# Kernel optimization log

Hardware: AMD Instinct MI355X
Metric: run time of the kernel (lower is better)

The kernel has to match this reference:

```python
import jax, jax.numpy as jnp
import numpy as np

B, S, HID = 2, 2048, 2048
NH, NKV, D = 32, 8, 64
G = NH // NKV
THETA = 150000.0


def rotate_half(x):
    x1, x2 = x[..., : D // 2], x[..., D // 2 :]
    return jnp.concatenate([-x2, x1], axis=-1)


def setup_inputs() -> dict:
    key = jax.random.key(0)
    ks = jax.random.split(key, 10)
    sc = 0.02
    return {
        "hidden_states": jax.random.normal(ks[0], (B, S, HID), jnp.float32),
        "position_ids": jnp.arange(S, dtype=jnp.int64 if jax.config.jax_enable_x64 else jnp.int32),
        "wq": jax.random.normal(ks[1], (HID, NH * D), jnp.float32) * sc,
        "bq": jax.random.normal(ks[2], (NH * D,), jnp.float32) * sc,
        "wk": jax.random.normal(ks[3], (HID, NKV * D), jnp.float32) * sc,
        "bk": jax.random.normal(ks[4], (NKV * D,), jnp.float32) * sc,
        "wv": jax.random.normal(ks[5], (HID, NKV * D), jnp.float32) * sc,
        "bv": jax.random.normal(ks[6], (NKV * D,), jnp.float32) * sc,
        "wo": jax.random.normal(ks[7], (NH * D, HID), jnp.float32) * sc,
        "bo": jax.random.normal(ks[8], (HID,), jnp.float32) * sc,
    }


def reference(hidden_states, position_ids, wq, bq, wk, bk, wv, bv, wo, bo):
    # projections: [B,S,NH,D] / [B,S,NKV,D] -> head-major
    q = (hidden_states @ wq + bq).reshape(B, S, NH, D).transpose(0, 2, 1, 3)   # [B,NH,S,D]
    k = (hidden_states @ wk + bk).reshape(B, S, NKV, D).transpose(0, 2, 1, 3)  # [B,NKV,S,D]
    v = (hidden_states @ wv + bv).reshape(B, S, NKV, D).transpose(0, 2, 1, 3)

    # HF RoPE: inv_freq over even dims, freqs duplicated across the two halves
    inv_freq = 1.0 / (THETA ** (jnp.arange(0, D, 2, dtype=jnp.float32) / D))   # [D/2]
    freqs = position_ids.astype(jnp.float32)[:, None] * inv_freq[None, :]      # [S,D/2]
    emb = jnp.concatenate([freqs, freqs], axis=-1)                             # [S,D]
    cos = jnp.cos(emb)[None, None]  # [1,1,S,D]
    sin = jnp.sin(emb)[None, None]
    q = q * cos + rotate_half(q) * sin
    k = k * cos + rotate_half(k) * sin

    # GQA: group query heads by kv head instead of repeat_interleave on K/V
    qg = q.reshape(B, NKV, G, S, D)
    scores = jnp.einsum("bkgsd,bktd->bkgst", qg, k) / jnp.sqrt(jnp.float32(D))  # [B,NKV,G,S,S]
    attn = jax.nn.softmax(scores, axis=-1)
    out = jnp.einsum("bkgst,bktd->bkgsd", attn, v)                              # [B,NKV,G,S,D]
    out = out.reshape(B, NH, S, D).transpose(0, 2, 1, 3).reshape(B, S, NH * D)  # [B,S,NH*D]
    return out @ wo + bo
```

## Files before the change

kernel.cpp:

```cpp
#include <hip/hip_runtime.h>
#include <hip/hip_bf16.h>
#include <math.h>

#define B_   2
#define S_   2048
#define HID_ 2048
#define NH_  32
#define NKV_ 8
#define D_   64
#define G_   (NH_/NKV_)
#define M_   (B_*S_)

typedef __hip_bfloat16 bf16;
typedef short bf16x8 __attribute__((ext_vector_type(8)));
typedef float f32x4  __attribute__((ext_vector_type(4)));
typedef unsigned short u16x4 __attribute__((ext_vector_type(4)));

__device__ inline unsigned short f2bfu(float f){
    __hip_bfloat16 h = __float2bfloat16(f);
    return __builtin_bit_cast(unsigned short, h);
}

__device__ __forceinline__ float fexp2(float x){
#if __has_builtin(__builtin_amdgcn_exp2f)
    return __builtin_amdgcn_exp2f(x);
#else
    return exp2f(x);
#endif
}

__device__ __forceinline__ void async16(const void* g, void* l) {
    __builtin_amdgcn_global_load_lds(
        (const __attribute__((address_space(1))) unsigned int*)g,
        (__attribute__((address_space(3))) unsigned int*)l, 16, 0, 0);
}

#define SWZ(r, c) ((c) ^ (((r) & 7) << 3))

#define S_BARRIER() asm volatile("s_barrier" ::: "memory")
__device__ __forceinline__ void vmwait4(){ asm volatile("s_waitcnt vmcnt(4)" ::: "memory"); }
__device__ __forceinline__ void vmwait0(){ asm volatile("s_waitcnt vmcnt(0)" ::: "memory"); }

__device__ __forceinline__ void wtrans_body(
    const float* __restrict__ s0, int N0,
    const float* __restrict__ s1, int N1,
    const float* __restrict__ s2, int N2,
    bf16* __restrict__ dst, int K, int bx, int by,
    unsigned short* __restrict__ tbuf)
{
    unsigned short (*t)[65] = (unsigned short (*)[65])tbuf;
    const int ntile = bx * 64, ktile = by * 64;
    const float* src; int nloc, Nseg;
    if (ntile < N0)           { src = s0; nloc = ntile;           Nseg = N0; }
    else if (ntile < N0 + N1) { src = s1; nloc = ntile - N0;      Nseg = N1; }
    else                      { src = s2; nloc = ntile - N0 - N1; Nseg = N2; }
    const int r  = threadIdx.x >> 4;
    const int c4 = (threadIdx.x & 15) * 4;
    #pragma unroll
    for (int p = 0; p < 4; p++) {
        const int k = p * 16 + r;
        const float4 f = *(const float4*)(src + (size_t)(ktile + k) * Nseg + nloc + c4);
        t[k][c4+0] = f2bfu(f.x); t[k][c4+1] = f2bfu(f.y);
        t[k][c4+2] = f2bfu(f.z); t[k][c4+3] = f2bfu(f.w);
    }
    __syncthreads();
    #pragma unroll
    for (int p = 0; p < 4; p++) {
        const int n = p * 16 + r;
        u16x4 u = { t[c4+0][n], t[c4+1][n], t[c4+2][n], t[c4+3][n] };
        *(u16x4*)((unsigned short*)dst + (size_t)(ntile + n) * K + ktile + c4) = u;
    }
}

__global__ __launch_bounds__(256) void prep_k(
    const float* __restrict__ hs, bf16* __restrict__ hs_b,
    const float* __restrict__ wq, const float* __restrict__ wk,
    const float* __restrict__ wv, bf16* __restrict__ wqkvT,
    const int* __restrict__ pos, float* __restrict__ ctab,
    float* __restrict__ stab)
{
    __shared__ unsigned short tbuf[64 * 65];
    const int bid = blockIdx.x;
    if (bid < 4096) {
        const int i = (bid * 256 + threadIdx.x) * 8;
        const float4 a = *(const float4*)(hs + i);
        const float4 b = *(const float4*)(hs + i + 4);
        uint4 u;
        u.x = (unsigned)f2bfu(a.x) | ((unsigned)f2bfu(a.y) << 16);
        u.y = (unsigned)f2bfu(a.z) | ((unsigned)f2bfu(a.w) << 16);
        u.z = (unsigned)f2bfu(b.x) | ((unsigned)f2bfu(b.y) << 16);
        u.w = (unsigned)f2bfu(b.z) | ((unsigned)f2bfu(b.w) << 16);
        *(uint4*)((unsigned short*)hs_b + i) = u;
    } else if (bid < 5632) {
        const int t = bid - 4096;
        wtrans_body(wq, 2048, wk, 512, wv, 512, wqkvT, HID_,
                    t % 48, t / 48, tbuf);
    } else {
        const int idx = (bid - 5632) * 256 + threadIdx.x;
        const int s = idx >> 5, i = idx & 31;
        const int is64 = (pos[1] == 0);
        const int p = is64 ? pos[2 * s] : pos[s];
        const double inv = exp(-(double)i * (log(150000.0) / 32.0));
        const double f = (double)p * inv;
        ctab[idx] = (float)cos(f);
        stab[idx] = (float)sin(f);
    }
}

__device__ __forceinline__ void slab64(
    const bf16* __restrict__ g, int grow0, int k0,
    unsigned short* lds, int wave, int lane)
{
    const int rr = wave * 8 + (lane >> 3);
    const int cc = ((lane & 7) ^ (lane >> 3)) * 8;
    async16(g + (size_t)(grow0 + rr) * 2048 + k0 + cc, lds + wave * 512);
}

template<int MODE, int BM>
__global__ __launch_bounds__(512, 2) void gemm8p_k(
    const bf16* __restrict__ A, const bf16* __restrict__ WT,
    const float* __restrict__ b0, const float* __restrict__ b1,
    const float* __restrict__ b2,
    bf16* __restrict__ Cq, bf16* __restrict__ Ck, bf16* __restrict__ Cv,
    float* __restrict__ Cout,
    const float* __restrict__ ctab, const float* __restrict__ stab)
{
    constexpr int MT = BM / 32;
    constexpr int PM = MT / 4;
    constexpr int LA = BM * 64;
    constexpr int LB = 256 * 64;
    constexpr int NT = 32;
    __shared__ unsigned short sA[2 * LA];
    __shared__ unsigned short sB[2 * LB];

    const int tid  = threadIdx.x;
    const int wave = tid >> 6, lane = tid & 63;
    const int li   = lane & 15, lj = lane >> 4;
    const int wm   = wave >> 2, wn = wave & 3;

    const int nbx = gridDim.x, nby = gridDim.y;
    const int lin = blockIdx.y * nbx + blockIdx.x;
    const int qq  = (nbx * nby) >> 3;
    const int logical = (lin & 7) * qq + (lin >> 3);
    const int m0 = (logical % nby) * BM;
    const int n0 = (logical / nby) * 256;
    const int swz = li & 7;

    f32x4 acc[MT][4];
    #pragma unroll
    for (int i = 0; i < MT; ++i)
        #pragma unroll
        for (int j = 0; j < 4; ++j)
            acc[i][j] = (f32x4){0.f, 0.f, 0.f, 0.f};

    bf16x8 bfr[4][2];

    auto stageA = [&](int t, int r0) {
        unsigned short* l = sA + (t & 1) * LA + r0 * 64;
        const int k0 = (t & (NT - 1)) * 64;
        slab64(A, m0 + r0,      k0, l,           wave, lane);
        slab64(A, m0 + r0 + 64, k0, l + 64 * 64, wave, lane);
    };
    auto stageB = [&](int t, int r0) {
        unsigned short* l = sB + (t & 1) * LB + r0 * 64;
        const int k0 = (t & (NT - 1)) * 64;
        slab64(WT, n0 + r0,      k0, l,           wave, lane);
        slab64(WT, n0 + r0 + 64, k0, l + 64 * 64, wave, lane);
    };
    auto ldB = [&](int tb) {
        const unsigned short* base = sB + tb * LB;
        #pragma unroll
        for (int nt = 0; nt < 4; ++nt)
            #pragma unroll
            for (int ks = 0; ks < 2; ++ks)
                bfr[nt][ks] = *(const bf16x8*)
                    &base[(wn * 64 + nt * 16 + li) * 64 + ((ks * 4 + lj) ^ swz) * 8];
    };
    auto ldA = [&](int tb, int q, bf16x8 (*af)[2]) {
        const unsigned short* base = sA + tb * LA;
        #pragma unroll
        for (int m = 0; m < PM; ++m)
            #pragma unroll
            for (int ks = 0; ks < 2; ++ks)
                af[m][ks] = *(const bf16x8*)
                    &base[(wm * (BM / 2) + (q * PM + m) * 16 + li) * 64
                          + ((ks * 4 + lj) ^ swz) * 8];
    };
    auto mfma_q = [&](int q, bf16x8 (*af)[2]) {
        __builtin_amdgcn_s_setprio(1);
        #pragma unroll
        for (int ks = 0; ks < 2; ++ks)
            #pragma unroll
            for (int m = 0; m < PM; ++m)
                #pragma unroll
                for (int nt = 0; nt < 4; ++nt)
                    acc[q * PM + m][nt] = __builtin_amdgcn_mfma_f32_16x16x32_bf16(
                        af[m][ks], bfr[nt][ks], acc[q * PM + m][nt], 0, 0, 0);
        __builtin_amdgcn_s_setprio(0);
    };

    stageA(0, 0);
    if constexpr (BM == 256) stageA(0, 128);
    stageB(0, 0); stageB(0, 128);
    stageB(1, 0); stageB(1, 128);
    vmwait4();
    S_BARRIER();

    for (int i = 0; i < NT / 2; ++i) {
        const int ta = 2 * i, tb = 2 * i + 1;
        bf16x8 af0[PM][2], af1[PM][2], af2[PM][2], af3[PM][2];
        ldB(0); ldA(0, 0, af0);
        stageA(tb, 0);
        S_BARRIER(); mfma_q(0, af0); S_BARRIER();
        ldA(0, 1, af1);
        if constexpr (BM == 256) stageA(tb, 128);
        S_BARRIER(); mfma_q(1, af1); S_BARRIER();
        ldA(0, 2, af2);
        stageB(ta + 2, 0);
        S_BARRIER(); mfma_q(2, af2); S_BARRIER();
        ldA(0, 3, af3);
        stageB(ta + 2, 128);
        S_BARRIER(); mfma_q(3, af3);
        vmwait4();
        S_BARRIER();
        ldB(1); ldA(1, 0, af0);
        stageA(ta + 2, 0);
        S_BARRIER(); mfma_q(0, af0); S_BARRIER();
        ldA(1, 1, af1);
        if constexpr (BM == 256) stageA(ta + 2, 128);
        S_BARRIER(); mfma_q(1, af1); S_BARRIER();
        ldA(1, 2, af2);
        stageB(tb + 2, 0);
        S_BARRIER(); mfma_q(2, af2); S_BARRIER();
        ldA(1, 3, af3);
        stageB(tb + 2, 128);
        S_BARRIER(); mfma_q(3, af3);
        vmwait4();
        S_BARRIER();
    }
    vmwait0();
    S_BARRIER();

    if (MODE == 1) {
        #pragma unroll
        for (int mt = 0; mt < MT; ++mt)
            #pragma unroll
            for (int nt = 0; nt < 4; ++nt) {
                const int col = n0 + wn * 64 + nt * 16 + li;
                const float bb = b0[col];
                #pragma unroll
                for (int r = 0; r < 4; ++r) {
                    const int row = m0 + wm * (BM / 2) + mt * 16 + lj * 4 + r;
                    Cout[(size_t)row * HID_ + col] = acc[mt][nt][r] + bb;
                }
            }
        return;
    }

    int seg, cb; const float* bias;
    if (n0 < 2048)      { seg = 0; cb = n0;        bias = b0; }
    else if (n0 < 2560) { seg = 1; cb = n0 - 2048; bias = b1; }
    else                { seg = 2; cb = n0 - 2560; bias = b2; }

    float bl[4];
    #pragma unroll
    for (int nt = 0; nt < 4; ++nt) bl[nt] = bias[cb + wn * 64 + nt * 16 + li];

    if (seg == 2) {
        const int b = m0 >> 11;
        #pragma unroll
        for (int nt = 0; nt < 4; ++nt) {
            const int cseg = cb + wn * 64 + nt * 16 + li;
            const int hv = cseg >> 6, d = cseg & 63;
            #pragma unroll
            for (int mt = 0; mt < MT; ++mt) {
                const int sb = (m0 & (S_ - 1)) + wm * (BM / 2) + mt * 16 + lj * 4;
                u16x4 u = { f2bfu(acc[mt][nt][0] + bl[nt]),
                            f2bfu(acc[mt][nt][1] + bl[nt]),
                            f2bfu(acc[mt][nt][2] + bl[nt]),
                            f2bfu(acc[mt][nt][3] + bl[nt]) };
                *(u16x4*)((unsigned short*)Cv +
                    ((size_t)((b * NKV_ + hv) * 64 + d)) * S_ + sb) = u;
            }
        }
        return;
    }

    const float qs = (seg == 0) ? 0.18033688011112042f : 1.0f;
    #pragma unroll
    for (int mt = 0; mt < MT; ++mt) {
        #pragma unroll
        for (int r = 0; r < 4; ++r) {
            const int row = m0 + wm * (BM / 2) + mt * 16 + lj * 4 + r;
            const int s = row & (S_ - 1);
            const float c0  = ctab[s * 32 + li],      sn0 = stab[s * 32 + li];
            const float c1  = ctab[s * 32 + 16 + li], sn1 = stab[s * 32 + 16 + li];
            const float x0 = acc[mt][0][r] + bl[0];
            const float x1 = acc[mt][1][r] + bl[1];
            const float x2 = acc[mt][2][r] + bl[2];
            const float x3 = acc[mt][3][r] + bl[3];
            const float y0 = (x0 * c0 - x2 * sn0) * qs;
            const float y2 = (x2 * c0 + x0 * sn0) * qs;
            const float y1 = (x1 * c1 - x3 * sn1) * qs;
            const float y3 = (x3 * c1 + x1 * sn1) * qs;
            if (seg == 0) {
                bf16* cp = Cq + (size_t)row * HID_ + n0 + wn * 64 + li;
                cp[0]  = __float2bfloat16(y0);
                cp[16] = __float2bfloat16(y1);
                cp[32] = __float2bfloat16(y2);
                cp[48] = __float2bfloat16(y3);
            } else {
                bf16* cp = Ck + (size_t)row * 512 + cb + wn * 64 + li;
                cp[0]  = __float2bfloat16(y0);
                cp[16] = __float2bfloat16(y1);
                cp[32] = __float2bfloat16(y2);
                cp[48] = __float2bfloat16(y3);
            }
        }
    }
}

__global__ __launch_bounds__(256, 4) void attn_k(
    const bf16* __restrict__ qws, const bf16* __restrict__ kws,
    const bf16* __restrict__ vtw, bf16* __restrict__ ows,
    const float* __restrict__ wo, bf16* __restrict__ woT)
{
    __shared__ unsigned short sMem[16384];

    if (blockIdx.y >= 64) {
        const int t = (blockIdx.y - 64) * 16 + blockIdx.x;
        wtrans_body(wo, 2048, wo, 0, wo, 0, woT, HID_, t & 31, t >> 5, sMem);
        return;
    }

    unsigned short* sK  = sMem;
    unsigned short* sVt = sMem + 4096;
    unsigned short* sP  = sMem + 8192;

    const int tid  = threadIdx.x;
    const int wave = tid >> 6, lane = tid & 63;
    const int li   = lane & 15, lj = lane >> 4;
    const int bh   = blockIdx.y;
    const int q0   = blockIdx.x * 128;
    const int b    = bh / NH_, h = bh % NH_;
    const int hk   = h / G_;

    bf16x8 qf[2][2];
    #pragma unroll
    for (int g = 0; g < 2; g++) {
        const bf16* qp = qws + (size_t)(b * S_ + q0 + wave * 32 + g * 16 + li) * HID_
                         + h * D_ + lj * 8;
        qf[g][0] = *(const bf16x8*)(qp);
        qf[g][1] = *(const bf16x8*)(qp + 32);
    }

    f32x4 o[2][4];
    #pragma unroll
    for (int g = 0; g < 2; g++)
        #pragma unroll
        for (int mt = 0; mt < 4; mt++) o[g][mt] = (f32x4){0.f, 0.f, 0.f, 0.f};
    float mr[2] = {-1e30f, -1e30f};
    float ll[2] = {0.f, 0.f};

    const int srow = tid >> 2, scol = (tid & 3) * 16;
    const bf16* kb = kws + (size_t)b * S_ * 512 + hk * 64;
    const bf16* vb = vtw + (size_t)((b * NKV_ + hk) * 64) * S_;
    unsigned short* sp = sP + wave * (32 * 64);

    uint4 pk0, pk1, pv0, pv1;
    {
        const uint4* kp = (const uint4*)(kb + (size_t)srow * 512 + scol);
        const uint4* vp = (const uint4*)(vb + (size_t)srow * S_ + scol);
        pk0 = kp[0]; pk1 = kp[1]; pv0 = vp[0]; pv1 = vp[1];
    }

    for (int kt = 0; kt < S_; kt += 64) {
        __syncthreads();
        *(uint4*)&sK [srow * 64 + SWZ(srow, scol)]     = pk0;
        *(uint4*)&sK [srow * 64 + SWZ(srow, scol + 8)] = pk1;
        *(uint4*)&sVt[srow * 64 + SWZ(srow, scol)]     = pv0;
        *(uint4*)&sVt[srow * 64 + SWZ(srow, scol + 8)] = pv1;
        __syncthreads();

        if (kt + 64 < S_) {
            const uint4* kp = (const uint4*)(kb + (size_t)(kt + 64 + srow) * 512 + scol);
            const uint4* vp = (const uint4*)(vb + (size_t)srow * S_ + kt + 64 + scol);
            pk0 = kp[0]; pk1 = kp[1]; pv0 = vp[0]; pv1 = vp[1];
        }

        float sc[2][4][4];
        __builtin_amdgcn_s_setprio(1);
        #pragma unroll
        for (int nt = 0; nt < 4; nt++) {
            f32x4 c0 = (f32x4){0.f, 0.f, 0.f, 0.f};
            f32x4 c1 = (f32x4){0.f, 0.f, 0.f, 0.f};
            #pragma unroll
            for (int ks = 0; ks < 2; ks++) {
                const bf16x8 kf =
                    *(const bf16x8*)&sK[(nt * 16 + li) * 64 + SWZ(li, ks * 32 + lj * 8)];
                c0 = __builtin_amdgcn_mfma_f32_16x16x32_bf16(kf, qf[0][ks], c0, 0, 0, 0);
                c1 = __builtin_amdgcn_mfma_f32_16x16x32_bf16(kf, qf[1][ks], c1, 0, 0, 0);
            }
            #pragma unroll
            for (int r = 0; r < 4; r++) { sc[0][nt][r] = c0[r]; sc[1][nt][r] = c1[r]; }
        }
        __builtin_amdgcn_s_setprio(0);

        #pragma unroll
        for (int g = 0; g < 2; g++) {
            float cm = sc[g][0][0];
            #pragma unroll
            for (int nt = 0; nt < 4; nt++)
                #pragma unroll
                for (int r = 0; r < 4; r++) cm = fmaxf(cm, sc[g][nt][r]);
            cm = fmaxf(cm, __shfl_xor(cm, 16));
            cm = fmaxf(cm, __shfl_xor(cm, 32));
            if (!__all(cm - mr[g] <= 8.0f)) {
                const float mnew = fmaxf(mr[g], cm);
                const float al   = fexp2(mr[g] - mnew);
                mr[g] = mnew;
                ll[g] *= al;
                #pragma unroll
                for (int mt = 0; mt < 4; mt++) o[g][mt] *= al;
            }
            float rs = 0.f;
            #pragma unroll
            for (int nt = 0; nt < 4; nt++) {
                const float e0 = fexp2(sc[g][nt][0] - mr[g]);
                const float e1 = fexp2(sc[g][nt][1] - mr[g]);
                const float e2 = fexp2(sc[g][nt][2] - mr[g]);
                const float e3 = fexp2(sc[g][nt][3] - mr[g]);
                rs += (e0 + e1) + (e2 + e3);
                u16x4 u = { f2bfu(e0), f2bfu(e1), f2bfu(e2), f2bfu(e3) };
                *(u16x4*)&sp[(g * 16 + li) * 64 + SWZ(li, nt * 16 + lj * 4)] = u;
            }
            ll[g] += rs;
        }

        __builtin_amdgcn_s_setprio(1);
        #pragma unroll
        for (int ks = 0; ks < 2; ks++) {
            const bf16x8 pf0 = *(const bf16x8*)&sp[(li)      * 64 + SWZ(li, ks * 32 + lj * 8)];
            const bf16x8 pf1 = *(const bf16x8*)&sp[(16 + li) * 64 + SWZ(li, ks * 32 + lj * 8)];
            #pragma unroll
            for (int mt = 0; mt < 4; mt++) {
                const bf16x8 vf =
                    *(const bf16x8*)&sVt[(mt * 16 + li) * 64 + SWZ(li, ks * 32 + lj * 8)];
                o[0][mt] = __builtin_amdgcn_mfma_f32_16x16x32_bf16(vf, pf0, o[0][mt], 0, 0, 0);
                o[1][mt] = __builtin_amdgcn_mfma_f32_16x16x32_bf16(vf, pf1, o[1][mt], 0, 0, 0);
            }
        }
        __builtin_amdgcn_s_setprio(0);
    }

    #pragma unroll
    for (int g = 0; g < 2; g++) {
        float l = ll[g];
        l += __shfl_xor(l, 16);
        l += __shfl_xor(l, 32);
        const float inv = 1.0f / l;
        bf16* op = ows + (size_t)(b * S_ + q0 + wave * 32 + g * 16 + li) * HID_ + h * D_;
        #pragma unroll
        for (int mt = 0; mt < 4; mt++) {
            u16x4 u = { f2bfu(o[g][mt][0] * inv), f2bfu(o[g][mt][1] * inv),
                        f2bfu(o[g][mt][2] * inv), f2bfu(o[g][mt][3] * inv) };
            *(u16x4*)((unsigned short*)op + mt * 16 + lj * 4) = u;
        }
    }
}

extern "C" void kernel_launch(void* const* d_in, const int* in_sizes, int n_in,
                              void* d_out, int out_size, void* d_ws, size_t ws_size,
                              hipStream_t stream)
{
    const float* hs  = (const float*)d_in[0];
    const int*   pos = (const int*)d_in[1];
    const float* wq = (const float*)d_in[2];
    const float* bq = (const float*)d_in[3];
    const float* wk = (const float*)d_in[4];
    const float* bk = (const float*)d_in[5];
    const float* wv = (const float*)d_in[6];
    const float* bv = (const float*)d_in[7];
    const float* wo = (const float*)d_in[8];
    const float* bo = (const float*)d_in[9];

    char* ws = (char*)d_ws;
    float* ctab  = (float*)(ws);
    float* stab  = (float*)(ws + (256u << 10));
    bf16*  k_ws  = (bf16*)(ws + (512u << 10));
    bf16*  v_t   = (bf16*)(ws + (512u << 10) + (4u  << 20));
    bf16*  q_ws  = (bf16*)(ws + (512u << 10) + (8u  << 20));
    bf16*  hs_b  = (bf16*)(ws + (512u << 10) + (24u << 20));
    bf16*  o_ws  = hs_b;
    bf16*  wqkvT = (bf16*)(ws + (512u << 10) + (40u << 20));
    bf16*  woT   = wqkvT;

    prep_k<<<dim3(5888), dim3(256), 0, stream>>>(
        hs, hs_b, wq, wk, wv, wqkvT, pos, ctab, stab);

    gemm8p_k<0, 256><<<dim3(12, 16), dim3(512), 0, stream>>>(
        hs_b, wqkvT, bq, bk, bv, q_ws, k_ws, v_t, nullptr, ctab, stab);

    attn_k<<<dim3(16, 128), dim3(256), 0, stream>>>(
        q_ws, k_ws, v_t, o_ws, wo, woT);

    gemm8p_k<1, 128><<<dim3(8, 32), dim3(512), 0, stream>>>(
        o_ws, woT, bo, nullptr, nullptr, nullptr, nullptr, nullptr,
        (float*)d_out, nullptr, nullptr);
}
```

Before: 325.0 us.

## Double attention query tile per block and reuse K/V fragments from registers

Each attention block now covers 256 query rows instead of 128, so each wave handles four 16-row groups. K and V^T fragments are loaded from LDS into registers once per key tile and reused across all four groups. This halves K/V global and LDS traffic per query row. In exchange, register pressure and LDS use grow, the launch bound drops to 2 blocks per CU, and the grid of attention blocks is halved, which can leave fewer waves to hide latency. The wo-transpose block indexing is adjusted so it still covers the same 1024 tiles.

```diff
diff --git a/kernel.cpp b/kernel.cpp
--- a/kernel.cpp
+++ b/kernel.cpp
@@ -320,15 +320,15 @@
     }
 }
 
-__global__ __launch_bounds__(256, 4) void attn_k(
+__global__ __launch_bounds__(256, 2) void attn_k(
     const bf16* __restrict__ qws, const bf16* __restrict__ kws,
     const bf16* __restrict__ vtw, bf16* __restrict__ ows,
     const float* __restrict__ wo, bf16* __restrict__ woT)
 {
-    __shared__ unsigned short sMem[16384];
+    __shared__ unsigned short sMem[24576];
 
     if (blockIdx.y >= 64) {
-        const int t = (blockIdx.y - 64) * 16 + blockIdx.x;
+        const int t = (blockIdx.y - 64) * 8 + blockIdx.x;
         wtrans_body(wo, 2048, wo, 0, wo, 0, woT, HID_, t & 31, t >> 5, sMem);
         return;
     }
@@ -341,31 +341,31 @@
     const int wave = tid >> 6, lane = tid & 63;
     const int li   = lane & 15, lj = lane >> 4;
     const int bh   = blockIdx.y;
-    const int q0   = blockIdx.x * 128;
+    const int q0   = blockIdx.x * 256;
     const int b    = bh / NH_, h = bh % NH_;
     const int hk   = h / G_;
 
-    bf16x8 qf[2][2];
-    #pragma unroll
-    for (int g = 0; g < 2; g++) {
-        const bf16* qp = qws + (size_t)(b * S_ + q0 + wave * 32 + g * 16 + li) * HID_
+    bf16x8 qf[4][2];
+    #pragma unroll
+    for (int g = 0; g < 4; g++) {
+        const bf16* qp = qws + (size_t)(b * S_ + q0 + wave * 64 + g * 16 + li) * HID_
                          + h * D_ + lj * 8;
         qf[g][0] = *(const bf16x8*)(qp);
         qf[g][1] = *(const bf16x8*)(qp + 32);
     }
 
-    f32x4 o[2][4];
-    #pragma unroll
-    for (int g = 0; g < 2; g++)
+    f32x4 o[4][4];
+    #pragma unroll
+    for (int g = 0; g < 4; g++)
         #pragma unroll
         for (int mt = 0; mt < 4; mt++) o[g][mt] = (f32x4){0.f, 0.f, 0.f, 0.f};
-    float mr[2] = {-1e30f, -1e30f};
-    float ll[2] = {0.f, 0.f};
+    float mr[4] = {-1e30f, -1e30f, -1e30f, -1e30f};
+    float ll[4] = {0.f, 0.f, 0.f, 0.f};
 
     const int srow = tid >> 2, scol = (tid & 3) * 16;
     const bf16* kb = kws + (size_t)b * S_ * 512 + hk * 64;
     const bf16* vb = vtw + (size_t)((b * NKV_ + hk) * 64) * S_;
-    unsigned short* sp = sP + wave * (32 * 64);
+    unsigned short* sp = sP + wave * (64 * 64);
 
     uint4 pk0, pk1, pv0, pv1;
     {
@@ -388,31 +388,33 @@
             pk0 = kp[0]; pk1 = kp[1]; pv0 = vp[0]; pv1 = vp[1];
         }
 
-        float sc[2][4][4];
-        __builtin_amdgcn_s_setprio(1);
-        #pragma unroll
-        for (int nt = 0; nt < 4; nt++) {
-            f32x4 c0 = (f32x4){0.f, 0.f, 0.f, 0.f};
-            f32x4 c1 = (f32x4){0.f, 0.f, 0.f, 0.f};
-            #pragma unroll
-            for (int ks = 0; ks < 2; ks++) {
-                const bf16x8 kf =
-                    *(const bf16x8*)&sK[(nt * 16 + li) * 64 + SWZ(li, ks * 32 + lj * 8)];
-                c0 = __builtin_amdgcn_mfma_f32_16x16x32_bf16(kf, qf[0][ks], c0, 0, 0, 0);
-                c1 = __builtin_amdgcn_mfma_f32_16x16x32_bf16(kf, qf[1][ks], c1, 0, 0, 0);
-            }
-            #pragma unroll
-            for (int r = 0; r < 4; r++) { sc[0][nt][r] = c0[r]; sc[1][nt][r] = c1[r]; }
-        }
-        __builtin_amdgcn_s_setprio(0);
-
-        #pragma unroll
-        for (int g = 0; g < 2; g++) {
-            float cm = sc[g][0][0];
+        bf16x8 kf[4][2];
+        #pragma unroll
+        for (int nt = 0; nt < 4; nt++)
+            #pragma unroll
+            for (int ks = 0; ks < 2; ks++)
+                kf[nt][ks] = *(const bf16x8*)&sK[(nt * 16 + li) * 64
+                                                 + SWZ(li, ks * 32 + lj * 8)];
+
+        #pragma unroll
+        for (int g = 0; g < 4; g++) {
+            f32x4 c[4];
+            __builtin_amdgcn_s_setprio(1);
+            #pragma unroll
+            for (int nt = 0; nt < 4; nt++) {
+                c[nt] = (f32x4){0.f, 0.f, 0.f, 0.f};
+                #pragma unroll
+                for (int ks = 0; ks < 2; ks++)
+                    c[nt] = __builtin_amdgcn_mfma_f32_16x16x32_bf16(
+                        kf[nt][ks], qf[g][ks], c[nt], 0, 0, 0);
+            }
+            __builtin_amdgcn_s_setprio(0);
+
+            float cm = c[0][0];
             #pragma unroll
             for (int nt = 0; nt < 4; nt++)
                 #pragma unroll
-                for (int r = 0; r < 4; r++) cm = fmaxf(cm, sc[g][nt][r]);
+                for (int r = 0; r < 4; r++) cm = fmaxf(cm, c[nt][r]);
             cm = fmaxf(cm, __shfl_xor(cm, 16));
             cm = fmaxf(cm, __shfl_xor(cm, 32));
             if (!__all(cm - mr[g] <= 8.0f)) {
@@ -426,10 +428,10 @@
             float rs = 0.f;
             #pragma unroll
             for (int nt = 0; nt < 4; nt++) {
-                const float e0 = fexp2(sc[g][nt][0] - mr[g]);
-                const float e1 = fexp2(sc[g][nt][1] - mr[g]);
-                const float e2 = fexp2(sc[g][nt][2] - mr[g]);
-                const float e3 = fexp2(sc[g][nt][3] - mr[g]);
+                const float e0 = fexp2(c[nt][0] - mr[g]);
+                const float e1 = fexp2(c[nt][1] - mr[g]);
+                const float e2 = fexp2(c[nt][2] - mr[g]);
+                const float e3 = fexp2(c[nt][3] - mr[g]);
                 rs += (e0 + e1) + (e2 + e3);
                 u16x4 u = { f2bfu(e0), f2bfu(e1), f2bfu(e2), f2bfu(e3) };
                 *(u16x4*)&sp[(g * 16 + li) * 64 + SWZ(li, nt * 16 + lj * 4)] = u;
@@ -437,29 +439,37 @@
             ll[g] += rs;
         }
 
+        bf16x8 vf[4][2];
+        #pragma unroll
+        for (int mt = 0; mt < 4; mt++)
+            #pragma unroll
+            for (int ks = 0; ks < 2; ks++)
+                vf[mt][ks] = *(const bf16x8*)&sVt[(mt * 16 + li) * 64
+                                                  + SWZ(li, ks * 32 + lj * 8)];
+
         __builtin_amdgcn_s_setprio(1);
         #pragma unroll
-        for (int ks = 0; ks < 2; ks++) {
-            const bf16x8 pf0 = *(const bf16x8*)&sp[(li)      * 64 + SWZ(li, ks * 32 + lj * 8)];
-            const bf16x8 pf1 = *(const bf16x8*)&sp[(16 + li) * 64 + SWZ(li, ks * 32 + lj * 8)];
-            #pragma unroll
-            for (int mt = 0; mt < 4; mt++) {
-                const bf16x8 vf =
-                    *(const bf16x8*)&sVt[(mt * 16 + li) * 64 + SWZ(li, ks * 32 + lj * 8)];
-                o[0][mt] = __builtin_amdgcn_mfma_f32_16x16x32_bf16(vf, pf0, o[0][mt], 0, 0, 0);
-                o[1][mt] = __builtin_amdgcn_mfma_f32_16x16x32_bf16(vf, pf1, o[1][mt], 0, 0, 0);
+        for (int g = 0; g < 4; g++) {
+            #pragma unroll
+            for (int ks = 0; ks < 2; ks++) {
+                const bf16x8 pf = *(const bf16x8*)&sp[(g * 16 + li) * 64
+                                                      + SWZ(li, ks * 32 + lj * 8)];
+                #pragma unroll
+                for (int mt = 0; mt < 4; mt++)
+                    o[g][mt] = __builtin_amdgcn_mfma_f32_16x16x32_bf16(
+                        vf[mt][ks], pf, o[g][mt], 0, 0, 0);
             }
         }
         __builtin_amdgcn_s_setprio(0);
     }
 
     #pragma unroll
-    for (int g = 0; g < 2; g++) {
+    for (int g = 0; g < 4; g++) {
         float l = ll[g];
         l += __shfl_xor(l, 16);
         l += __shfl_xor(l, 32);
         const float inv = 1.0f / l;
-        bf16* op = ows + (size_t)(b * S_ + q0 + wave * 32 + g * 16 + li) * HID_ + h * D_;
+        bf16* op = ows + (size_t)(b * S_ + q0 + wave * 64 + g * 16 + li) * HID_ + h * D_;
         #pragma unroll
         for (int mt = 0; mt < 4; mt++) {
             u16x4 u = { f2bfu(o[g][mt][0] * inv), f2bfu(o[g][mt][1] * inv),
@@ -501,7 +511,7 @@
     gemm8p_k<0, 256><<<dim3(12, 16), dim3(512), 0, stream>>>(
         hs_b, wqkvT, bq, bk, bv, q_ws, k_ws, v_t, nullptr, ctab, stab);
 
-    attn_k<<<dim3(16, 128), dim3(256), 0, stream>>>(
+    attn_k<<<dim3(8, 192), dim3(256), 0, stream>>>(
         q_ws, k_ws, v_t, o_ws, wo, woT);
 
     gemm8p_k<1, 128><<<dim3(8, 32), dim3(512), 0, stream>>>(
```

Result: no change. 321.0 us (-1.2%).
